# Kernel tuning notes

Hardware: AMD Instinct MI355X
Metric: run time of the kernel (lower is better)

Reference implementation:

```python
import jax, jax.numpy as jnp
import numpy as np

N, E, H, IN, OUT, A, L = 20000, 320000, 128, 16, 16, 4, 4
EPS = 1e-5


def _ln(x, g, b):
    mu = jnp.mean(x, axis=-1, keepdims=True)
    v = jnp.mean((x - mu) ** 2, axis=-1, keepdims=True)
    return (x - mu) * jax.lax.rsqrt(v + EPS) * g + b


def setup_inputs() -> dict:
    key = jax.random.key(0)
    ks = jax.random.split(key, 24)
    x = jax.random.normal(ks[0], (N, 3), dtype=jnp.float32)
    h = jax.random.normal(ks[1], (N, IN), dtype=jnp.float32)
    src = jax.random.randint(ks[2], (E,), 0, N)
    src = src.at[:N].set(jnp.arange(N))  # ensure every node has out-degree>=1 so c>0
    dst = jax.random.randint(ks[3], (E,), 0, N)
    edges = jnp.stack([src, dst]).astype(jnp.int32)
    edge_attr = jax.random.normal(ks[4], (E, A), dtype=jnp.float32)
    s = 0.05
    d_in = 2 * H + 1 + A
    p = {
        "emb_w": jax.random.normal(ks[5], (IN, H)) * s, "emb_b": jnp.zeros((H,)),
        "out_w": jax.random.normal(ks[6], (H, OUT)) * s, "out_b": jnp.zeros((OUT,)),
        "pe_w1": jax.random.normal(ks[7], (L, d_in, H)) * s, "pe_b1": jnp.zeros((L, H)),
        "pe_g1": jnp.ones((L, H)), "pe_bb1": jnp.zeros((L, H)),
        "pe_w2": jax.random.normal(ks[8], (L, H, H)) * s, "pe_b2": jnp.zeros((L, H)),
        "pe_g2": jnp.ones((L, H)), "pe_bb2": jnp.zeros((L, H)),
        "px_w1": jax.random.normal(ks[9], (L, H, H)) * s, "px_b1": jnp.zeros((L, H)),
        "px_g1": jnp.ones((L, H)), "px_bb1": jnp.zeros((L, H)),
        "px_w2": jax.random.normal(ks[10], (L, H, 1)) * s, "px_b2": jnp.zeros((L, 1)),
        "ph_w1": jax.random.normal(ks[11], (L, 2 * H, H)) * s, "ph_b1": jnp.zeros((L, H)),
        "ph_g1": jnp.ones((L, H)), "ph_bb1": jnp.zeros((L, H)),
        "ph_w2": jax.random.normal(ks[12], (L, H, H)) * s, "ph_b2": jnp.zeros((L, H)),
    }
    out = {"x": x, "h": h, "edges": edges, "edge_attr": edge_attr}
    out.update(p)
    return out


def reference(x, h, edges, edge_attr, emb_w, emb_b, out_w, out_b,
              pe_w1, pe_b1, pe_g1, pe_bb1, pe_w2, pe_b2, pe_g2, pe_bb2,
              px_w1, px_b1, px_g1, px_bb1, px_w2, px_b2,
              ph_w1, ph_b1, ph_g1, ph_bb1, ph_w2, ph_b2):
    n = x.shape[0]
    j, i = edges[0], edges[1]  # PyG: x_j = source, x_i = target; aggregate at target i
    # c = in-neighborhood size computed from edge_index[0] (as in the original code)
    c = jax.ops.segment_sum(jnp.ones((edges.shape[1],), x.dtype), j, num_segments=n)[:, None]
    h = h @ emb_w + emb_b
    for l in range(L):
        d = x[i] - x[j]                                   # [E,3]
        d2 = jnp.sum(d * d, axis=-1, keepdims=True)       # ||x_i - x_j||^2
        m_in = jnp.concatenate([h[i], h[j], d2, edge_attr], axis=-1)
        t = jax.nn.silu(_ln(m_in @ pe_w1[l] + pe_b1[l], pe_g1[l], pe_bb1[l]))
        mh = jax.nn.silu(_ln(t @ pe_w2[l] + pe_b2[l], pe_g2[l], pe_bb2[l]))  # [E,H]
        t2 = jax.nn.silu(_ln(mh @ px_w1[l] + px_b1[l], px_g1[l], px_bb1[l]))
        mx = d * (t2 @ px_w2[l] + px_b2[l])               # [E,3]
        agg_x = jax.ops.segment_sum(mx, i, num_segments=n)
        agg_h = jax.ops.segment_sum(mh, i, num_segments=n)
        u = jnp.concatenate([h, agg_h], axis=-1)
        t3 = jax.nn.silu(_ln(u @ ph_w1[l] + ph_b1[l], ph_g1[l], ph_bb1[l]))
        h = t3 @ ph_w2[l] + ph_b2[l] + h                  # ResWrapper residual
        x = x + agg_x / c
    h = h @ out_w + out_b
    return (x, h)
```

## Files before the change

### kernel.cpp

```cpp
#include <hip/hip_runtime.h>

#define NN 20000
#define NE 320000
#define HD 128
#define IND 16
#define OUTD 16
#define NL 4
#define LN_EPS 1e-5f
#define LDA 136

typedef __attribute__((ext_vector_type(8))) short bf16x8;
typedef __attribute__((ext_vector_type(4))) float f32x4;

__device__ __forceinline__ unsigned short f2b(float f) {
  union { float f; unsigned int u; } v; v.f = f;
  unsigned int r = v.u + 0x7FFFu + ((v.u >> 16) & 1u);
  return (unsigned short)(r >> 16);
}
__device__ __forceinline__ float b2f(unsigned int lo16) {
  union { unsigned int u; float f; } v; v.u = lo16 << 16; return v.f;
}


__global__ void prep_zero_k(const float* __restrict__ xin, float* __restrict__ xf,
                            float* __restrict__ cnt, int* __restrict__ deg) {
  int i = blockIdx.x * 256 + threadIdx.x;
  if (i < NN * 3) xf[i] = xin[i];
  if (i < NN) { cnt[i] = 0.f; deg[i] = 0; }
}

__global__ void count_k(const int* __restrict__ edges, float* __restrict__ cnt,
                        int* __restrict__ deg) {
  int e = blockIdx.x * 256 + threadIdx.x;
  if (e < NE) {
    atomicAdd(&cnt[edges[e]], 1.f);
    atomicAdd(&deg[edges[NE + e]], 1);
  }
}

__global__ void inv_k(float* __restrict__ cnt) {
  int n = blockIdx.x * 256 + threadIdx.x;
  if (n < NN) { float c = cnt[n]; cnt[n] = (c > 0.f) ? 1.f / c : 0.f; }
}

__global__ void scan_k(const int* __restrict__ deg, int* __restrict__ rowptr,
                       int* __restrict__ cursor) {
  __shared__ int part[256];
  const int tid = threadIdx.x;
  const int base = tid * 79;
  int s = 0;
  for (int t = 0; t < 79; ++t) { int idx = base + t; if (idx < NN) s += deg[idx]; }
  part[tid] = s;
  __syncthreads();
  for (int off = 1; off < 256; off <<= 1) {
    int v = (tid >= off) ? part[tid - off] : 0;
    __syncthreads();
    part[tid] += v;
    __syncthreads();
  }
  int run = (tid == 0) ? 0 : part[tid - 1];
  for (int t = 0; t < 79; ++t) {
    int idx = base + t;
    if (idx < NN) { rowptr[idx] = run; cursor[idx] = run; run += deg[idx]; }
  }
  if (tid == 255) rowptr[NN] = run;
}

__global__ void scatter_k(const int* __restrict__ edges, int* __restrict__ cursor,
                          int* __restrict__ eids) {
  int e = blockIdx.x * 256 + threadIdx.x;
  if (e < NE) {
    int d = edges[NE + e];
    int pos = atomicAdd(&cursor[d], 1);
    eids[pos] = e;
  }
}

__global__ void prep_w_k(const float* __restrict__ src, unsigned short* __restrict__ dst,
                         int KT, int Kreal) {
  int i = blockIdx.x * 256 + threadIdx.x;
  int total = NL * KT * 4096;
  if (i >= total) return;
  int kk = i & 31;
  int c = (i >> 5) & 127;
  int lkt = i >> 12;
  int kt = lkt % KT;
  int l = lkt / KT;
  int k = kt * 32 + kk;
  float v = (k < Kreal) ? src[((size_t)l * Kreal + k) * HD + c] : 0.f;
  dst[i] = f2b(v);
}

__global__ void emb_k(const float* __restrict__ hin, const float* __restrict__ w,
                      const float* __restrict__ b, float* __restrict__ hf,
                      unsigned short* __restrict__ hb) {
  int i = blockIdx.x * 256 + threadIdx.x;
  if (i >= NN * HD) return;
  int n = i >> 7, c = i & 127;
  float acc = b[c];
#pragma unroll
  for (int k = 0; k < IND; ++k) acc += hin[n * IND + k] * w[k * HD + c];
  hf[i] = acc;
  hb[i] = f2b(acc);
}

__global__ void prepd_k(const float* __restrict__ xf, const int* __restrict__ edges,
                        const float* __restrict__ ea, float* __restrict__ dvec,
                        unsigned short* __restrict__ e8) {
  int e = blockIdx.x * 256 + threadIdx.x;
  if (e >= NE) return;
  int j = edges[e], i = edges[NE + e];
  float dx = xf[i * 3 + 0] - xf[j * 3 + 0];
  float dy = xf[i * 3 + 1] - xf[j * 3 + 1];
  float dz = xf[i * 3 + 2] - xf[j * 3 + 2];
  float d2 = dx * dx + dy * dy + dz * dz;
  dvec[e * 4 + 0] = dx; dvec[e * 4 + 1] = dy; dvec[e * 4 + 2] = dz; dvec[e * 4 + 3] = d2;
  e8[e * 8 + 0] = f2b(d2);
#pragma unroll
  for (int a = 0; a < 4; ++a) e8[e * 8 + 1 + a] = f2b(ea[e * 4 + a]);
  e8[e * 8 + 5] = 0; e8[e * 8 + 6] = 0; e8[e * 8 + 7] = 0;
}

__global__ void outproj_k(const float* __restrict__ hf, const float* __restrict__ w,
                          const float* __restrict__ b, float* __restrict__ out) {
  int i = blockIdx.x * 256 + threadIdx.x;
  if (i >= NN * OUTD) return;
  int n = i >> 4, o = i & 15;
  float acc = b[o];
#pragma unroll 8
  for (int k = 0; k < HD; ++k) acc += hf[(size_t)n * HD + k] * w[k * OUTD + o];
  out[NN * 3 + i] = acc;
}

__global__ void xcopy_k(const float* __restrict__ xf, float* __restrict__ out) {
  int i = blockIdx.x * 256 + threadIdx.x;
  if (i < NN * 3) out[i] = xf[i];
}


__global__ __launch_bounds__(256) void gather_k(const unsigned short* __restrict__ tbuf,
                                                const float* __restrict__ sc,
                                                const float* __restrict__ dvec,
                                                const int* __restrict__ rowptr,
                                                const int* __restrict__ eids,
                                                const float* __restrict__ cinv,
                                                float* __restrict__ aggh,
                                                float* __restrict__ xf) {
  const int n = blockIdx.x * 4 + (threadIdx.x >> 6);
  if (n >= NN) return;
  const int lane = threadIdx.x & 63;
  const int s = rowptr[n], e = rowptr[n + 1];
  float a0 = 0.f, a1 = 0.f, xa = 0.f;
  for (int t = s; t < e; ++t) {
    const int eid = eids[t];
    const unsigned int v = *(const unsigned int*)(tbuf + (size_t)eid * HD + lane * 2);
    a0 += b2f(v & 0xffffu);
    a1 += b2f(v >> 16);
    if (lane < 3) xa += dvec[(size_t)eid * 4 + lane] * sc[eid];
  }
  aggh[(size_t)n * HD + lane * 2] = a0;
  aggh[(size_t)n * HD + lane * 2 + 1] = a1;
  if (lane < 3) xf[n * 3 + lane] += xa * cinv[n];
}


__device__ __forceinline__ void mfma16(const bf16x8 (&af)[4], const bf16x8 (&bq)[4],
                                       f32x4 (&acc)[4][4]) {
#pragma unroll
  for (int mf = 0; mf < 4; ++mf)
#pragma unroll
    for (int nf = 0; nf < 4; ++nf)
      acc[mf][nf] = __builtin_amdgcn_mfma_f32_16x16x32_bf16(af[mf], bq[nf], acc[mf][nf], 0, 0, 0);
}

__device__ __forceinline__ void ln_silu(f32x4 (&acc)[4][4], float (*lnb)[128][2],
                                        const float* bias, const float* g, const float* bb,
                                        int wm, int wn, int lid, int q) {
  float biasc[4], gc[4], bbc[4];
#pragma unroll
  for (int nf = 0; nf < 4; ++nf) {
    const int c = wn * 64 + nf * 16 + lid;
    biasc[nf] = bias[c]; gc[nf] = g[c]; bbc[nf] = bb[c];
  }
#pragma unroll
  for (int mf = 0; mf < 4; ++mf)
#pragma unroll
    for (int nf = 0; nf < 4; ++nf)
#pragma unroll
      for (int rg = 0; rg < 4; ++rg) acc[mf][nf][rg] += biasc[nf];

  float s_[4][4], ss_[4][4];
#pragma unroll
  for (int mf = 0; mf < 4; ++mf)
#pragma unroll
    for (int rg = 0; rg < 4; ++rg) {
      float a = 0.f, b = 0.f;
#pragma unroll
      for (int nf = 0; nf < 4; ++nf) { float v = acc[mf][nf][rg]; a += v; b += v * v; }
      s_[mf][rg] = a; ss_[mf][rg] = b;
    }
#pragma unroll
  for (int m = 1; m < 16; m <<= 1) {
#pragma unroll
    for (int mf = 0; mf < 4; ++mf)
#pragma unroll
      for (int rg = 0; rg < 4; ++rg) {
        s_[mf][rg] += __shfl_xor(s_[mf][rg], m);
        ss_[mf][rg] += __shfl_xor(ss_[mf][rg], m);
      }
  }
  if (lid == 0) {
#pragma unroll
    for (int mf = 0; mf < 4; ++mf)
#pragma unroll
      for (int rg = 0; rg < 4; ++rg) {
        const int rl = wm * 64 + mf * 16 + q * 4 + rg;
        lnb[wn][rl][0] = s_[mf][rg];
        lnb[wn][rl][1] = ss_[mf][rg];
      }
  }
  __syncthreads();
#pragma unroll
  for (int mf = 0; mf < 4; ++mf)
#pragma unroll
    for (int rg = 0; rg < 4; ++rg) {
      const int rl = wm * 64 + mf * 16 + q * 4 + rg;
      const float t0 = lnb[0][rl][0] + lnb[1][rl][0];
      const float t1 = lnb[0][rl][1] + lnb[1][rl][1];
      const float mu = t0 * (1.f / HD);
      const float var = t1 * (1.f / HD) - mu * mu;
      const float rstd = rsqrtf(var + LN_EPS);
#pragma unroll
      for (int nf = 0; nf < 4; ++nf) {
        float v = acc[mf][nf][rg];
        v = (v - mu) * rstd * gc[nf] + bbc[nf];
        acc[mf][nf][rg] = v / (1.f + __expf(-v));
      }
    }
}

__device__ __forceinline__ void write_tile(const f32x4 (&acc)[4][4], unsigned short* At,
                                           int wm, int wn, int lid, int q) {
#pragma unroll
  for (int mf = 0; mf < 4; ++mf)
#pragma unroll
    for (int rg = 0; rg < 4; ++rg) {
      const int row = wm * 64 + mf * 16 + q * 4 + rg;
#pragma unroll
      for (int nf = 0; nf < 4; ++nf) {
        const int col = wn * 64 + nf * 16 + lid;
        At[row * LDA + col] = f2b(acc[mf][nf][rg]);
      }
    }
}


struct EP {
  const unsigned short* hb;
  const unsigned short* e8;
  const int* edges;
  const unsigned short *w1, *w2, *w3;
  const float *b1, *g1, *bb1, *b2, *g2, *bb2, *b3, *g3, *bb3;
  const float *w4, *b4;
  unsigned short* tbuf;
  float* sc;
};

__global__ __launch_bounds__(256, 2) void edge_k(EP p) {
  __shared__ __align__(16) unsigned short At[128 * LDA];
  __shared__ float lnb[2][2][128][2];

  const int tid = threadIdx.x, lane = tid & 63, lid = lane & 15, q = lane >> 4;
  const int wave = tid >> 6, wm = wave >> 1, wn = wave & 1;
  const int row0 = blockIdx.x * 128;

  int rowA[4], ei[4], ej[4], colB[4];
#pragma unroll
  for (int mf = 0; mf < 4; ++mf) {
    rowA[mf] = wm * 64 + mf * 16 + lid;
    ei[mf] = p.edges[NE + row0 + rowA[mf]];
    ej[mf] = p.edges[row0 + rowA[mf]];
  }
#pragma unroll
  for (int nf = 0; nf < 4; ++nf) colB[nf] = wn * 64 + nf * 16 + lid;

  const bf16x8 zv = {0, 0, 0, 0, 0, 0, 0, 0};

  auto ld1 = [&](int kt, bf16x8 (&A)[4], bf16x8 (&B)[4]) {
#pragma unroll
    for (int mf = 0; mf < 4; ++mf) {
      if (kt < 4)
        A[mf] = *(const bf16x8*)(p.hb + (size_t)ei[mf] * HD + kt * 32 + q * 8);
      else if (kt < 8)
        A[mf] = *(const bf16x8*)(p.hb + (size_t)ej[mf] * HD + (kt - 4) * 32 + q * 8);
      else if (q == 0)
        A[mf] = *(const bf16x8*)(p.e8 + (size_t)(row0 + rowA[mf]) * 8);
      else
        A[mf] = zv;
    }
#pragma unroll
    for (int nf = 0; nf < 4; ++nf)
      B[nf] = *(const bf16x8*)(p.w1 + (size_t)kt * 4096 + colB[nf] * 32 + q * 8);
  };
  auto ldL = [&](const unsigned short* wt, int kt, bf16x8 (&A)[4], bf16x8 (&B)[4]) {
#pragma unroll
    for (int mf = 0; mf < 4; ++mf)
      A[mf] = *(const bf16x8*)&At[rowA[mf] * LDA + kt * 32 + q * 8];
#pragma unroll
    for (int nf = 0; nf < 4; ++nf)
      B[nf] = *(const bf16x8*)(wt + (size_t)kt * 4096 + colB[nf] * 32 + q * 8);
  };

  f32x4 acc[4][4];
#pragma unroll
  for (int a = 0; a < 4; ++a)
#pragma unroll
    for (int b = 0; b < 4; ++b) acc[a][b] = (f32x4){0.f, 0.f, 0.f, 0.f};

  bf16x8 A0[4], B0[4], A1[4], B1[4], A2[4], B2[4];

  ld1(0, A0, B0); ld1(1, A1, B1);
  ld1(2, A2, B2); mfma16(A0, B0, acc);
  ld1(3, A0, B0); mfma16(A1, B1, acc);
  ld1(4, A1, B1); mfma16(A2, B2, acc);
  ld1(5, A2, B2); mfma16(A0, B0, acc);
  ld1(6, A0, B0); mfma16(A1, B1, acc);
  ld1(7, A1, B1); mfma16(A2, B2, acc);
  ld1(8, A2, B2); mfma16(A0, B0, acc);
  mfma16(A1, B1, acc);
  mfma16(A2, B2, acc);

  ln_silu(acc, lnb[0], p.b1, p.g1, p.bb1, wm, wn, lid, q);
  write_tile(acc, At, wm, wn, lid, q);
  __syncthreads();

#pragma unroll
  for (int a = 0; a < 4; ++a)
#pragma unroll
    for (int b = 0; b < 4; ++b) acc[a][b] = (f32x4){0.f, 0.f, 0.f, 0.f};
  ldL(p.w2, 0, A0, B0); ldL(p.w2, 1, A1, B1);
  ldL(p.w2, 2, A2, B2); mfma16(A0, B0, acc);
  ldL(p.w2, 3, A0, B0); mfma16(A1, B1, acc);
  mfma16(A2, B2, acc);
  mfma16(A0, B0, acc);

  ln_silu(acc, lnb[1], p.b2, p.g2, p.bb2, wm, wn, lid, q);
  write_tile(acc, At, wm, wn, lid, q);
  __syncthreads();

#pragma unroll
  for (int c4 = 0; c4 < 8; ++c4) {
    const int idx = tid + c4 * 256;
    const int row = idx >> 4, sl = idx & 15;
    const uint4 v = *(const uint4*)&At[row * LDA + sl * 8];
    *(uint4*)(p.tbuf + (size_t)(row0 + row) * HD + sl * 8) = v;
  }

#pragma unroll
  for (int a = 0; a < 4; ++a)
#pragma unroll
    for (int b = 0; b < 4; ++b) acc[a][b] = (f32x4){0.f, 0.f, 0.f, 0.f};
  ldL(p.w3, 0, A0, B0); ldL(p.w3, 1, A1, B1);
  ldL(p.w3, 2, A2, B2); mfma16(A0, B0, acc);
  ldL(p.w3, 3, A0, B0); mfma16(A1, B1, acc);
  mfma16(A2, B2, acc);
  mfma16(A0, B0, acc);

  ln_silu(acc, lnb[0], p.b3, p.g3, p.bb3, wm, wn, lid, q);

  float w4c[4];
#pragma unroll
  for (int nf = 0; nf < 4; ++nf) w4c[nf] = p.w4[colB[nf]];
  float dp[4][4];
#pragma unroll
  for (int mf = 0; mf < 4; ++mf)
#pragma unroll
    for (int rg = 0; rg < 4; ++rg) {
      float a = 0.f;
#pragma unroll
      for (int nf = 0; nf < 4; ++nf) a += acc[mf][nf][rg] * w4c[nf];
      dp[mf][rg] = a;
    }
#pragma unroll
  for (int m = 1; m < 16; m <<= 1) {
#pragma unroll
    for (int mf = 0; mf < 4; ++mf)
#pragma unroll
      for (int rg = 0; rg < 4; ++rg) dp[mf][rg] += __shfl_xor(dp[mf][rg], m);
  }
  if (lid == 0) {
#pragma unroll
    for (int mf = 0; mf < 4; ++mf)
#pragma unroll
      for (int rg = 0; rg < 4; ++rg)
        lnb[1][wn][wm * 64 + mf * 16 + q * 4 + rg][0] = dp[mf][rg];
  }
  __syncthreads();
  if (tid < 128) p.sc[row0 + tid] = lnb[1][0][tid][0] + lnb[1][1][tid][0] + p.b4[0];
}


struct NP {
  const float* hf;
  const float* aggh;
  const unsigned short *w4t, *w5t;
  const float *b1, *g1, *bb1, *b5;
  float* hf_out;
  unsigned short* hb_out;
};

__global__ __launch_bounds__(256, 2) void node_k(NP p) {
  __shared__ __align__(16) unsigned short At[128 * LDA];
  __shared__ float lnb[1][2][128][2];

  const int tid = threadIdx.x, lane = tid & 63, lid = lane & 15, q = lane >> 4;
  const int wave = tid >> 6, wm = wave >> 1, wn = wave & 1;
  const int row0 = blockIdx.x * 128;

  int rowA[4], nrow[4], colB[4];
  bool okm[4];
#pragma unroll
  for (int mf = 0; mf < 4; ++mf) {
    rowA[mf] = wm * 64 + mf * 16 + lid;
    nrow[mf] = row0 + rowA[mf];
    okm[mf] = nrow[mf] < NN;
  }
#pragma unroll
  for (int nf = 0; nf < 4; ++nf) colB[nf] = wn * 64 + nf * 16 + lid;

  const bf16x8 zv = {0, 0, 0, 0, 0, 0, 0, 0};

  auto ld4 = [&](int kt, bf16x8 (&A)[4], bf16x8 (&B)[4]) {
#pragma unroll
    for (int mf = 0; mf < 4; ++mf) {
      if (!okm[mf]) { A[mf] = zv; continue; }
      const float* s = (kt < 4) ? (p.hf + (size_t)nrow[mf] * HD + kt * 32 + q * 8)
                                : (p.aggh + (size_t)nrow[mf] * HD + (kt - 4) * 32 + q * 8);
      const float4 f0 = *(const float4*)s;
      const float4 f1 = *(const float4*)(s + 4);
      unsigned short t[8];
      t[0] = f2b(f0.x); t[1] = f2b(f0.y); t[2] = f2b(f0.z); t[3] = f2b(f0.w);
      t[4] = f2b(f1.x); t[5] = f2b(f1.y); t[6] = f2b(f1.z); t[7] = f2b(f1.w);
      A[mf] = *(const bf16x8*)t;
    }
#pragma unroll
    for (int nf = 0; nf < 4; ++nf)
      B[nf] = *(const bf16x8*)(p.w4t + (size_t)kt * 4096 + colB[nf] * 32 + q * 8);
  };
  auto ld5 = [&](int kt, bf16x8 (&A)[4], bf16x8 (&B)[4]) {
#pragma unroll
    for (int mf = 0; mf < 4; ++mf)
      A[mf] = *(const bf16x8*)&At[rowA[mf] * LDA + kt * 32 + q * 8];
#pragma unroll
    for (int nf = 0; nf < 4; ++nf)
      B[nf] = *(const bf16x8*)(p.w5t + (size_t)kt * 4096 + colB[nf] * 32 + q * 8);
  };

  f32x4 acc[4][4];
#pragma unroll
  for (int a = 0; a < 4; ++a)
#pragma unroll
    for (int b = 0; b < 4; ++b) acc[a][b] = (f32x4){0.f, 0.f, 0.f, 0.f};

  bf16x8 A0[4], B0[4], A1[4], B1[4], A2[4], B2[4];

  ld4(0, A0, B0); ld4(1, A1, B1);
  ld4(2, A2, B2); mfma16(A0, B0, acc);
  ld4(3, A0, B0); mfma16(A1, B1, acc);
  ld4(4, A1, B1); mfma16(A2, B2, acc);
  ld4(5, A2, B2); mfma16(A0, B0, acc);
  ld4(6, A0, B0); mfma16(A1, B1, acc);
  ld4(7, A1, B1); mfma16(A2, B2, acc);
  mfma16(A0, B0, acc);
  mfma16(A1, B1, acc);

  ln_silu(acc, lnb[0], p.b1, p.g1, p.bb1, wm, wn, lid, q);
  write_tile(acc, At, wm, wn, lid, q);
  __syncthreads();

#pragma unroll
  for (int a = 0; a < 4; ++a)
#pragma unroll
    for (int b = 0; b < 4; ++b) acc[a][b] = (f32x4){0.f, 0.f, 0.f, 0.f};
  ld5(0, A0, B0); ld5(1, A1, B1);
  ld5(2, A2, B2); mfma16(A0, B0, acc);
  ld5(3, A0, B0); mfma16(A1, B1, acc);
  mfma16(A2, B2, acc);
  mfma16(A0, B0, acc);

  float biasc[4];
#pragma unroll
  for (int nf = 0; nf < 4; ++nf) biasc[nf] = p.b5[colB[nf]];
#pragma unroll
  for (int mf = 0; mf < 4; ++mf)
#pragma unroll
    for (int rg = 0; rg < 4; ++rg) {
      const int row = wm * 64 + mf * 16 + q * 4 + rg;
      const int n = row0 + row;
      if (n < NN) {
#pragma unroll
        for (int nf = 0; nf < 4; ++nf) {
          const int c = colB[nf];
          const float v = acc[mf][nf][rg] + biasc[nf] + p.hf[(size_t)n * HD + c];
          p.hf_out[(size_t)n * HD + c] = v;
          p.hb_out[(size_t)n * HD + c] = f2b(v);
        }
      }
    }
}


extern "C" void kernel_launch(void* const* d_in, const int* in_sizes, int n_in,
                              void* d_out, int out_size, void* d_ws, size_t ws_size,
                              hipStream_t stream) {
  (void)in_sizes; (void)n_in; (void)out_size; (void)ws_size;
  const float* x_in = (const float*)d_in[0];
  const float* h_in = (const float*)d_in[1];
  const int* edges = (const int*)d_in[2];
  const float* eattr = (const float*)d_in[3];
  const float* emb_w = (const float*)d_in[4];
  const float* emb_b = (const float*)d_in[5];
  const float* out_w = (const float*)d_in[6];
  const float* out_b = (const float*)d_in[7];
  const float* pe_w1 = (const float*)d_in[8];
  const float* pe_b1 = (const float*)d_in[9];
  const float* pe_g1 = (const float*)d_in[10];
  const float* pe_bb1 = (const float*)d_in[11];
  const float* pe_w2 = (const float*)d_in[12];
  const float* pe_b2 = (const float*)d_in[13];
  const float* pe_g2 = (const float*)d_in[14];
  const float* pe_bb2 = (const float*)d_in[15];
  const float* px_w1 = (const float*)d_in[16];
  const float* px_b1 = (const float*)d_in[17];
  const float* px_g1 = (const float*)d_in[18];
  const float* px_bb1 = (const float*)d_in[19];
  const float* px_w2 = (const float*)d_in[20];
  const float* px_b2 = (const float*)d_in[21];
  const float* ph_w1 = (const float*)d_in[22];
  const float* ph_b1 = (const float*)d_in[23];
  const float* ph_g1 = (const float*)d_in[24];
  const float* ph_bb1 = (const float*)d_in[25];
  const float* ph_w2 = (const float*)d_in[26];
  const float* ph_b2 = (const float*)d_in[27];
  float* out = (float*)d_out;

  char* ws = (char*)d_ws;
  size_t off = 0;
  auto alloc = [&](size_t bytes) -> void* {
    void* ptr = ws + off;
    off = (off + bytes + 255) & ~(size_t)255;
    return ptr;
  };
  float* hf = (float*)alloc((size_t)NN * HD * 4);
  unsigned short* hb = (unsigned short*)alloc((size_t)NN * HD * 2);
  float* aggh = (float*)alloc((size_t)NN * HD * 4);
  float* xf = (float*)alloc((size_t)NN * 3 * 4);
  float* cinv = (float*)alloc((size_t)NN * 4);
  float* dvec = (float*)alloc((size_t)NE * 4 * 4);
  unsigned short* e8 = (unsigned short*)alloc((size_t)NE * 8 * 2);
  unsigned short* tbuf = (unsigned short*)alloc((size_t)NE * HD * 2);
  float* sc = (float*)alloc((size_t)NE * 4);
  int* deg = (int*)alloc((size_t)NN * 4);
  int* cursor = (int*)alloc((size_t)NN * 4);
  int* rowptr = (int*)alloc((size_t)(NN + 1) * 4);
  int* eids = (int*)alloc((size_t)NE * 4);
  unsigned short* w1t = (unsigned short*)alloc((size_t)NL * 9 * 4096 * 2);
  unsigned short* w2t = (unsigned short*)alloc((size_t)NL * 4 * 4096 * 2);
  unsigned short* w3t = (unsigned short*)alloc((size_t)NL * 4 * 4096 * 2);
  unsigned short* w4t = (unsigned short*)alloc((size_t)NL * 8 * 4096 * 2);
  unsigned short* w5t = (unsigned short*)alloc((size_t)NL * 4 * 4096 * 2);

  prep_zero_k<<<(NN * 3 + 255) / 256, 256, 0, stream>>>(x_in, xf, cinv, deg);
  count_k<<<(NE + 255) / 256, 256, 0, stream>>>(edges, cinv, deg);
  inv_k<<<(NN + 255) / 256, 256, 0, stream>>>(cinv);
  scan_k<<<1, 256, 0, stream>>>(deg, rowptr, cursor);
  scatter_k<<<(NE + 255) / 256, 256, 0, stream>>>(edges, cursor, eids);
  prep_w_k<<<(NL * 9 * 4096 + 255) / 256, 256, 0, stream>>>(pe_w1, w1t, 9, 261);
  prep_w_k<<<(NL * 4 * 4096 + 255) / 256, 256, 0, stream>>>(pe_w2, w2t, 4, 128);
  prep_w_k<<<(NL * 4 * 4096 + 255) / 256, 256, 0, stream>>>(px_w1, w3t, 4, 128);
  prep_w_k<<<(NL * 8 * 4096 + 255) / 256, 256, 0, stream>>>(ph_w1, w4t, 8, 256);
  prep_w_k<<<(NL * 4 * 4096 + 255) / 256, 256, 0, stream>>>(ph_w2, w5t, 4, 128);
  emb_k<<<(NN * HD + 255) / 256, 256, 0, stream>>>(h_in, emb_w, emb_b, hf, hb);

  const int egrid = NE / 128;
  const int ngrid = (NN + 127) / 128;

  for (int l = 0; l < NL; ++l) {
    prepd_k<<<(NE + 255) / 256, 256, 0, stream>>>(xf, edges, eattr, dvec, e8);
    {
      EP p{};
      p.hb = hb; p.e8 = e8; p.edges = edges;
      p.w1 = w1t + (size_t)l * 9 * 4096;
      p.w2 = w2t + (size_t)l * 4 * 4096;
      p.w3 = w3t + (size_t)l * 4 * 4096;
      p.b1 = pe_b1 + l * HD; p.g1 = pe_g1 + l * HD; p.bb1 = pe_bb1 + l * HD;
      p.b2 = pe_b2 + l * HD; p.g2 = pe_g2 + l * HD; p.bb2 = pe_bb2 + l * HD;
      p.b3 = px_b1 + l * HD; p.g3 = px_g1 + l * HD; p.bb3 = px_bb1 + l * HD;
      p.w4 = px_w2 + l * HD; p.b4 = px_b2 + l;
      p.tbuf = tbuf; p.sc = sc;
      edge_k<<<egrid, 256, 0, stream>>>(p);
    }
    gather_k<<<(NN + 3) / 4, 256, 0, stream>>>(tbuf, sc, dvec, rowptr, eids, cinv, aggh, xf);
    {
      NP p{};
      p.hf = hf; p.aggh = aggh;
      p.w4t = w4t + (size_t)l * 8 * 4096;
      p.w5t = w5t + (size_t)l * 4 * 4096;
      p.b1 = ph_b1 + l * HD; p.g1 = ph_g1 + l * HD; p.bb1 = ph_bb1 + l * HD;
      p.b5 = ph_b2 + l * HD;
      p.hf_out = hf; p.hb_out = hb;
      node_k<<<ngrid, 256, 0, stream>>>(p);
    }
  }

  outproj_k<<<(NN * OUTD + 255) / 256, 256, 0, stream>>>(hf, out_w, out_b, out);
  xcopy_k<<<(NN * 3 + 255) / 256, 256, 0, stream>>>(xf, out);
}
```

Before: 1.365 ms.

## Give each wave full-width row strips to drop cross-wave LayerNorm syncs

Switches the edge and node MLP kernels from a 2x2 wave tiling (64x64 per wave) to row strips where each wave owns 32 rows by all 128 columns. LayerNorm row statistics can then be reduced entirely within a wave, which removes the shared-memory reduction buffer and the block-wide barriers between the chained GEMMs. The GEMM pipeline moves from triple to double buffering, node_k now runs 128-thread blocks over 64 rows, and bf16 conversion now goes through the HIP intrinsic. The cost is that each wave loads the whole weight tile (8 B fragments per k-step instead of 4), so weight traffic per wave doubles and register pressure goes up.

```diff
diff --git a/kernel.cpp b/kernel.cpp
--- a/kernel.cpp
+++ b/kernel.cpp
@@ -1,4 +1,5 @@
 #include <hip/hip_runtime.h>
+#include <hip/hip_bf16.h>
 
 #define NN 20000
 #define NE 320000
@@ -13,9 +14,10 @@
 typedef __attribute__((ext_vector_type(4))) float f32x4;
 
 __device__ __forceinline__ unsigned short f2b(float f) {
-  union { float f; unsigned int u; } v; v.f = f;
-  unsigned int r = v.u + 0x7FFFu + ((v.u >> 16) & 1u);
-  return (unsigned short)(r >> 16);
+  __hip_bfloat16 h = __float2bfloat16(f);
+  unsigned short u;
+  __builtin_memcpy(&u, &h, 2);
+  return u;
 }
 __device__ __forceinline__ float b2f(unsigned int lo16) {
   union { unsigned int u; float f; } v; v.u = lo16 << 16; return v.f;
@@ -164,74 +166,76 @@
 }
 
 
-__device__ __forceinline__ void mfma16(const bf16x8 (&af)[4], const bf16x8 (&bq)[4],
-                                       f32x4 (&acc)[4][4]) {
-#pragma unroll
-  for (int mf = 0; mf < 4; ++mf)
-#pragma unroll
-    for (int nf = 0; nf < 4; ++nf)
-      acc[mf][nf] = __builtin_amdgcn_mfma_f32_16x16x32_bf16(af[mf], bq[nf], acc[mf][nf], 0, 0, 0);
-}
-
-__device__ __forceinline__ void ln_silu(f32x4 (&acc)[4][4], float (*lnb)[128][2],
-                                        const float* bias, const float* g, const float* bb,
-                                        int wm, int wn, int lid, int q) {
-  float biasc[4], gc[4], bbc[4];
-#pragma unroll
-  for (int nf = 0; nf < 4; ++nf) {
-    const int c = wn * 64 + nf * 16 + lid;
+__device__ __forceinline__ void mfma_w(const bf16x8 (&A)[2], const bf16x8 (&B)[8],
+                                       f32x4 (&acc)[2][8]) {
+#pragma unroll
+  for (int mf = 0; mf < 2; ++mf)
+#pragma unroll
+    for (int nf = 0; nf < 8; ++nf)
+      acc[mf][nf] = __builtin_amdgcn_mfma_f32_16x16x32_bf16(A[mf], B[nf], acc[mf][nf], 0, 0, 0);
+}
+
+#define ZACC()                                          \
+  _Pragma("unroll") for (int a_ = 0; a_ < 2; ++a_)      \
+  _Pragma("unroll") for (int b_ = 0; b_ < 8; ++b_)      \
+      acc[a_][b_] = (f32x4){0.f, 0.f, 0.f, 0.f}
+
+#define GEMM_PIPE(NKT, LD)                              \
+  LD(0, A0, B0);                                        \
+  _Pragma("unroll") for (int kt = 0; kt < (NKT); ++kt) {\
+    if ((kt & 1) == 0) {                                \
+      if (kt + 1 < (NKT)) LD(kt + 1, A1, B1);           \
+      mfma_w(A0, B0, acc);                              \
+    } else {                                            \
+      if (kt + 1 < (NKT)) LD(kt + 1, A0, B0);           \
+      mfma_w(A1, B1, acc);                              \
+    }                                                   \
+  }
+
+__device__ __forceinline__ void ln_silu_w(f32x4 (&acc)[2][8], const float* bias,
+                                          const float* g, const float* bb, int lid) {
+  float biasc[8], gc[8], bbc[8];
+#pragma unroll
+  for (int nf = 0; nf < 8; ++nf) {
+    const int c = nf * 16 + lid;
     biasc[nf] = bias[c]; gc[nf] = g[c]; bbc[nf] = bb[c];
   }
 #pragma unroll
-  for (int mf = 0; mf < 4; ++mf)
-#pragma unroll
-    for (int nf = 0; nf < 4; ++nf)
+  for (int mf = 0; mf < 2; ++mf)
+#pragma unroll
+    for (int nf = 0; nf < 8; ++nf)
 #pragma unroll
       for (int rg = 0; rg < 4; ++rg) acc[mf][nf][rg] += biasc[nf];
 
-  float s_[4][4], ss_[4][4];
-#pragma unroll
-  for (int mf = 0; mf < 4; ++mf)
+  float s_[2][4], ss_[2][4];
+#pragma unroll
+  for (int mf = 0; mf < 2; ++mf)
 #pragma unroll
     for (int rg = 0; rg < 4; ++rg) {
       float a = 0.f, b = 0.f;
 #pragma unroll
-      for (int nf = 0; nf < 4; ++nf) { float v = acc[mf][nf][rg]; a += v; b += v * v; }
+      for (int nf = 0; nf < 8; ++nf) { float v = acc[mf][nf][rg]; a += v; b += v * v; }
       s_[mf][rg] = a; ss_[mf][rg] = b;
     }
 #pragma unroll
   for (int m = 1; m < 16; m <<= 1) {
 #pragma unroll
-    for (int mf = 0; mf < 4; ++mf)
+    for (int mf = 0; mf < 2; ++mf)
 #pragma unroll
       for (int rg = 0; rg < 4; ++rg) {
         s_[mf][rg] += __shfl_xor(s_[mf][rg], m);
         ss_[mf][rg] += __shfl_xor(ss_[mf][rg], m);
       }
   }
-  if (lid == 0) {
-#pragma unroll
-    for (int mf = 0; mf < 4; ++mf)
-#pragma unroll
-      for (int rg = 0; rg < 4; ++rg) {
-        const int rl = wm * 64 + mf * 16 + q * 4 + rg;
-        lnb[wn][rl][0] = s_[mf][rg];
-        lnb[wn][rl][1] = ss_[mf][rg];
-      }
-  }
-  __syncthreads();
-#pragma unroll
-  for (int mf = 0; mf < 4; ++mf)
+#pragma unroll
+  for (int mf = 0; mf < 2; ++mf)
 #pragma unroll
     for (int rg = 0; rg < 4; ++rg) {
-      const int rl = wm * 64 + mf * 16 + q * 4 + rg;
-      const float t0 = lnb[0][rl][0] + lnb[1][rl][0];
-      const float t1 = lnb[0][rl][1] + lnb[1][rl][1];
-      const float mu = t0 * (1.f / HD);
-      const float var = t1 * (1.f / HD) - mu * mu;
+      const float mu = s_[mf][rg] * (1.f / HD);
+      const float var = ss_[mf][rg] * (1.f / HD) - mu * mu;
       const float rstd = rsqrtf(var + LN_EPS);
 #pragma unroll
-      for (int nf = 0; nf < 4; ++nf) {
+      for (int nf = 0; nf < 8; ++nf) {
         float v = acc[mf][nf][rg];
         v = (v - mu) * rstd * gc[nf] + bbc[nf];
         acc[mf][nf][rg] = v / (1.f + __expf(-v));
@@ -239,18 +243,16 @@
     }
 }
 
-__device__ __forceinline__ void write_tile(const f32x4 (&acc)[4][4], unsigned short* At,
-                                           int wm, int wn, int lid, int q) {
-#pragma unroll
-  for (int mf = 0; mf < 4; ++mf)
+__device__ __forceinline__ void write_strip(const f32x4 (&acc)[2][8], unsigned short* At,
+                                            int rbase, int lid, int q) {
+#pragma unroll
+  for (int mf = 0; mf < 2; ++mf)
 #pragma unroll
     for (int rg = 0; rg < 4; ++rg) {
-      const int row = wm * 64 + mf * 16 + q * 4 + rg;
-#pragma unroll
-      for (int nf = 0; nf < 4; ++nf) {
-        const int col = wn * 64 + nf * 16 + lid;
-        At[row * LDA + col] = f2b(acc[mf][nf][rg]);
-      }
+      const int row = rbase + mf * 16 + q * 4 + rg;
+#pragma unroll
+      for (int nf = 0; nf < 8; ++nf)
+        At[row * LDA + nf * 16 + lid] = f2b(acc[mf][nf][rg]);
     }
 }
 
@@ -268,135 +270,102 @@
 
 __global__ __launch_bounds__(256, 2) void edge_k(EP p) {
   __shared__ __align__(16) unsigned short At[128 * LDA];
-  __shared__ float lnb[2][2][128][2];
 
   const int tid = threadIdx.x, lane = tid & 63, lid = lane & 15, q = lane >> 4;
-  const int wave = tid >> 6, wm = wave >> 1, wn = wave & 1;
+  const int wave = tid >> 6;
+  const int rbase = wave * 32;
   const int row0 = blockIdx.x * 128;
 
-  int rowA[4], ei[4], ej[4], colB[4];
-#pragma unroll
-  for (int mf = 0; mf < 4; ++mf) {
-    rowA[mf] = wm * 64 + mf * 16 + lid;
-    ei[mf] = p.edges[NE + row0 + rowA[mf]];
-    ej[mf] = p.edges[row0 + rowA[mf]];
-  }
-#pragma unroll
-  for (int nf = 0; nf < 4; ++nf) colB[nf] = wn * 64 + nf * 16 + lid;
+  int ei[2], ej[2];
+#pragma unroll
+  for (int mf = 0; mf < 2; ++mf) {
+    const int r = row0 + rbase + mf * 16 + lid;
+    ei[mf] = p.edges[NE + r];
+    ej[mf] = p.edges[r];
+  }
 
   const bf16x8 zv = {0, 0, 0, 0, 0, 0, 0, 0};
 
-  auto ld1 = [&](int kt, bf16x8 (&A)[4], bf16x8 (&B)[4]) {
-#pragma unroll
-    for (int mf = 0; mf < 4; ++mf) {
+  auto LD1 = [&](int kt, bf16x8 (&A)[2], bf16x8 (&B)[8]) {
+#pragma unroll
+    for (int mf = 0; mf < 2; ++mf) {
       if (kt < 4)
         A[mf] = *(const bf16x8*)(p.hb + (size_t)ei[mf] * HD + kt * 32 + q * 8);
       else if (kt < 8)
         A[mf] = *(const bf16x8*)(p.hb + (size_t)ej[mf] * HD + (kt - 4) * 32 + q * 8);
       else if (q == 0)
-        A[mf] = *(const bf16x8*)(p.e8 + (size_t)(row0 + rowA[mf]) * 8);
+        A[mf] = *(const bf16x8*)(p.e8 + (size_t)(row0 + rbase + mf * 16 + lid) * 8);
       else
         A[mf] = zv;
     }
 #pragma unroll
-    for (int nf = 0; nf < 4; ++nf)
-      B[nf] = *(const bf16x8*)(p.w1 + (size_t)kt * 4096 + colB[nf] * 32 + q * 8);
+    for (int nf = 0; nf < 8; ++nf)
+      B[nf] = *(const bf16x8*)(p.w1 + (size_t)kt * 4096 + (nf * 16 + lid) * 32 + q * 8);
   };
-  auto ldL = [&](const unsigned short* wt, int kt, bf16x8 (&A)[4], bf16x8 (&B)[4]) {
-#pragma unroll
-    for (int mf = 0; mf < 4; ++mf)
-      A[mf] = *(const bf16x8*)&At[rowA[mf] * LDA + kt * 32 + q * 8];
-#pragma unroll
-    for (int nf = 0; nf < 4; ++nf)
-      B[nf] = *(const bf16x8*)(wt + (size_t)kt * 4096 + colB[nf] * 32 + q * 8);
+  auto LDW = [&](const unsigned short* wt, int kt, bf16x8 (&A)[2], bf16x8 (&B)[8]) {
+#pragma unroll
+    for (int mf = 0; mf < 2; ++mf)
+      A[mf] = *(const bf16x8*)&At[(rbase + mf * 16 + lid) * LDA + kt * 32 + q * 8];
+#pragma unroll
+    for (int nf = 0; nf < 8; ++nf)
+      B[nf] = *(const bf16x8*)(wt + (size_t)kt * 4096 + (nf * 16 + lid) * 32 + q * 8);
   };
-
-  f32x4 acc[4][4];
-#pragma unroll
-  for (int a = 0; a < 4; ++a)
-#pragma unroll
-    for (int b = 0; b < 4; ++b) acc[a][b] = (f32x4){0.f, 0.f, 0.f, 0.f};
-
-  bf16x8 A0[4], B0[4], A1[4], B1[4], A2[4], B2[4];
-
-  ld1(0, A0, B0); ld1(1, A1, B1);
-  ld1(2, A2, B2); mfma16(A0, B0, acc);
-  ld1(3, A0, B0); mfma16(A1, B1, acc);
-  ld1(4, A1, B1); mfma16(A2, B2, acc);
-  ld1(5, A2, B2); mfma16(A0, B0, acc);
-  ld1(6, A0, B0); mfma16(A1, B1, acc);
-  ld1(7, A1, B1); mfma16(A2, B2, acc);
-  ld1(8, A2, B2); mfma16(A0, B0, acc);
-  mfma16(A1, B1, acc);
-  mfma16(A2, B2, acc);
-
-  ln_silu(acc, lnb[0], p.b1, p.g1, p.bb1, wm, wn, lid, q);
-  write_tile(acc, At, wm, wn, lid, q);
-  __syncthreads();
-
-#pragma unroll
-  for (int a = 0; a < 4; ++a)
-#pragma unroll
-    for (int b = 0; b < 4; ++b) acc[a][b] = (f32x4){0.f, 0.f, 0.f, 0.f};
-  ldL(p.w2, 0, A0, B0); ldL(p.w2, 1, A1, B1);
-  ldL(p.w2, 2, A2, B2); mfma16(A0, B0, acc);
-  ldL(p.w2, 3, A0, B0); mfma16(A1, B1, acc);
-  mfma16(A2, B2, acc);
-  mfma16(A0, B0, acc);
-
-  ln_silu(acc, lnb[1], p.b2, p.g2, p.bb2, wm, wn, lid, q);
-  write_tile(acc, At, wm, wn, lid, q);
-  __syncthreads();
-
-#pragma unroll
-  for (int c4 = 0; c4 < 8; ++c4) {
-    const int idx = tid + c4 * 256;
+  auto LD2 = [&](int kt, bf16x8 (&A)[2], bf16x8 (&B)[8]) { LDW(p.w2, kt, A, B); };
+  auto LD3 = [&](int kt, bf16x8 (&A)[2], bf16x8 (&B)[8]) { LDW(p.w3, kt, A, B); };
+
+  f32x4 acc[2][8];
+  bf16x8 A0[2], B0[8], A1[2], B1[8];
+
+  ZACC();
+  GEMM_PIPE(9, LD1);
+  ln_silu_w(acc, p.b1, p.g1, p.bb1, lid);
+  write_strip(acc, At, rbase, lid, q);
+
+  ZACC();
+  GEMM_PIPE(4, LD2);
+  ln_silu_w(acc, p.b2, p.g2, p.bb2, lid);
+  write_strip(acc, At, rbase, lid, q);
+
+#pragma unroll
+  for (int it = 0; it < 8; ++it) {
+    const int idx = it * 64 + lane;
     const int row = idx >> 4, sl = idx & 15;
-    const uint4 v = *(const uint4*)&At[row * LDA + sl * 8];
-    *(uint4*)(p.tbuf + (size_t)(row0 + row) * HD + sl * 8) = v;
-  }
-
-#pragma unroll
-  for (int a = 0; a < 4; ++a)
-#pragma unroll
-    for (int b = 0; b < 4; ++b) acc[a][b] = (f32x4){0.f, 0.f, 0.f, 0.f};
-  ldL(p.w3, 0, A0, B0); ldL(p.w3, 1, A1, B1);
-  ldL(p.w3, 2, A2, B2); mfma16(A0, B0, acc);
-  ldL(p.w3, 3, A0, B0); mfma16(A1, B1, acc);
-  mfma16(A2, B2, acc);
-  mfma16(A0, B0, acc);
-
-  ln_silu(acc, lnb[0], p.b3, p.g3, p.bb3, wm, wn, lid, q);
-
-  float w4c[4];
-#pragma unroll
-  for (int nf = 0; nf < 4; ++nf) w4c[nf] = p.w4[colB[nf]];
-  float dp[4][4];
-#pragma unroll
-  for (int mf = 0; mf < 4; ++mf)
+    const uint4 v = *(const uint4*)&At[(rbase + row) * LDA + sl * 8];
+    *(uint4*)(p.tbuf + (size_t)(row0 + rbase + row) * HD + sl * 8) = v;
+  }
+
+  ZACC();
+  GEMM_PIPE(4, LD3);
+  ln_silu_w(acc, p.b3, p.g3, p.bb3, lid);
+
+  float w4c[8];
+#pragma unroll
+  for (int nf = 0; nf < 8; ++nf) w4c[nf] = p.w4[nf * 16 + lid];
+  float dp[2][4];
+#pragma unroll
+  for (int mf = 0; mf < 2; ++mf)
 #pragma unroll
     for (int rg = 0; rg < 4; ++rg) {
       float a = 0.f;
 #pragma unroll
-      for (int nf = 0; nf < 4; ++nf) a += acc[mf][nf][rg] * w4c[nf];
+      for (int nf = 0; nf < 8; ++nf) a += acc[mf][nf][rg] * w4c[nf];
       dp[mf][rg] = a;
     }
 #pragma unroll
   for (int m = 1; m < 16; m <<= 1) {
 #pragma unroll
-    for (int mf = 0; mf < 4; ++mf)
+    for (int mf = 0; mf < 2; ++mf)
 #pragma unroll
       for (int rg = 0; rg < 4; ++rg) dp[mf][rg] += __shfl_xor(dp[mf][rg], m);
   }
   if (lid == 0) {
-#pragma unroll
-    for (int mf = 0; mf < 4; ++mf)
+    const float b4 = p.b4[0];
+#pragma unroll
+    for (int mf = 0; mf < 2; ++mf)
 #pragma unroll
       for (int rg = 0; rg < 4; ++rg)
-        lnb[1][wn][wm * 64 + mf * 16 + q * 4 + rg][0] = dp[mf][rg];
-  }
-  __syncthreads();
-  if (tid < 128) p.sc[row0 + tid] = lnb[1][0][tid][0] + lnb[1][1][tid][0] + p.b4[0];
+        p.sc[row0 + rbase + mf * 16 + q * 4 + rg] = dp[mf][rg] + b4;
+  }
 }
 
 
@@ -409,30 +378,27 @@
   unsigned short* hb_out;
 };
 
-__global__ __launch_bounds__(256, 2) void node_k(NP p) {
-  __shared__ __align__(16) unsigned short At[128 * LDA];
-  __shared__ float lnb[1][2][128][2];
+__global__ __launch_bounds__(128, 2) void node_k(NP p) {
+  __shared__ __align__(16) unsigned short At[64 * LDA];
 
   const int tid = threadIdx.x, lane = tid & 63, lid = lane & 15, q = lane >> 4;
-  const int wave = tid >> 6, wm = wave >> 1, wn = wave & 1;
-  const int row0 = blockIdx.x * 128;
-
-  int rowA[4], nrow[4], colB[4];
-  bool okm[4];
-#pragma unroll
-  for (int mf = 0; mf < 4; ++mf) {
-    rowA[mf] = wm * 64 + mf * 16 + lid;
-    nrow[mf] = row0 + rowA[mf];
+  const int wave = tid >> 6;
+  const int rbase = wave * 32;
+  const int row0 = blockIdx.x * 64;
+
+  int nrow[2];
+  bool okm[2];
+#pragma unroll
+  for (int mf = 0; mf < 2; ++mf) {
+    nrow[mf] = row0 + rbase + mf * 16 + lid;
     okm[mf] = nrow[mf] < NN;
   }
-#pragma unroll
-  for (int nf = 0; nf < 4; ++nf) colB[nf] = wn * 64 + nf * 16 + lid;
 
   const bf16x8 zv = {0, 0, 0, 0, 0, 0, 0, 0};
 
-  auto ld4 = [&](int kt, bf16x8 (&A)[4], bf16x8 (&B)[4]) {
-#pragma unroll
-    for (int mf = 0; mf < 4; ++mf) {
+  auto LD4 = [&](int kt, bf16x8 (&A)[2], bf16x8 (&B)[8]) {
+#pragma unroll
+    for (int mf = 0; mf < 2; ++mf) {
       if (!okm[mf]) { A[mf] = zv; continue; }
       const float* s = (kt < 4) ? (p.hf + (size_t)nrow[mf] * HD + kt * 32 + q * 8)
                                 : (p.aggh + (size_t)nrow[mf] * HD + (kt - 4) * 32 + q * 8);
@@ -444,63 +410,41 @@
       A[mf] = *(const bf16x8*)t;
     }
 #pragma unroll
-    for (int nf = 0; nf < 4; ++nf)
-      B[nf] = *(const bf16x8*)(p.w4t + (size_t)kt * 4096 + colB[nf] * 32 + q * 8);
+    for (int nf = 0; nf < 8; ++nf)
+      B[nf] = *(const bf16x8*)(p.w4t + (size_t)kt * 4096 + (nf * 16 + lid) * 32 + q * 8);
   };
-  auto ld5 = [&](int kt, bf16x8 (&A)[4], bf16x8 (&B)[4]) {
-#pragma unroll
-    for (int mf = 0; mf < 4; ++mf)
-      A[mf] = *(const bf16x8*)&At[rowA[mf] * LDA + kt * 32 + q * 8];
-#pragma unroll
-    for (int nf = 0; nf < 4; ++nf)
-      B[nf] = *(const bf16x8*)(p.w5t + (size_t)kt * 4096 + colB[nf] * 32 + q * 8);
+  auto LD5 = [&](int kt, bf16x8 (&A)[2], bf16x8 (&B)[8]) {
+#pragma unroll
+    for (int mf = 0; mf < 2; ++mf)
+      A[mf] = *(const bf16x8*)&At[(rbase + mf * 16 + lid) * LDA + kt * 32 + q * 8];
+#pragma unroll
+    for (int nf = 0; nf < 8; ++nf)
+      B[nf] = *(const bf16x8*)(p.w5t + (size_t)kt * 4096 + (nf * 16 + lid) * 32 + q * 8);
   };
 
-  f32x4 acc[4][4];
-#pragma unroll
-  for (int a = 0; a < 4; ++a)
-#pragma unroll
-    for (int b = 0; b < 4; ++b) acc[a][b] = (f32x4){0.f, 0.f, 0.f, 0.f};
-
-  bf16x8 A0[4], B0[4], A1[4], B1[4], A2[4], B2[4];
-
-  ld4(0, A0, B0); ld4(1, A1, B1);
-  ld4(2, A2, B2); mfma16(A0, B0, acc);
-  ld4(3, A0, B0); mfma16(A1, B1, acc);
-  ld4(4, A1, B1); mfma16(A2, B2, acc);
-  ld4(5, A2, B2); mfma16(A0, B0, acc);
-  ld4(6, A0, B0); mfma16(A1, B1, acc);
-  ld4(7, A1, B1); mfma16(A2, B2, acc);
-  mfma16(A0, B0, acc);
-  mfma16(A1, B1, acc);
-
-  ln_silu(acc, lnb[0], p.b1, p.g1, p.bb1, wm, wn, lid, q);
-  write_tile(acc, At, wm, wn, lid, q);
-  __syncthreads();
-
-#pragma unroll
-  for (int a = 0; a < 4; ++a)
-#pragma unroll
-    for (int b = 0; b < 4; ++b) acc[a][b] = (f32x4){0.f, 0.f, 0.f, 0.f};
-  ld5(0, A0, B0); ld5(1, A1, B1);
-  ld5(2, A2, B2); mfma16(A0, B0, acc);
-  ld5(3, A0, B0); mfma16(A1, B1, acc);
-  mfma16(A2, B2, acc);
-  mfma16(A0, B0, acc);
-
-  float biasc[4];
-#pragma unroll
-  for (int nf = 0; nf < 4; ++nf) biasc[nf] = p.b5[colB[nf]];
-#pragma unroll
-  for (int mf = 0; mf < 4; ++mf)
+  f32x4 acc[2][8];
+  bf16x8 A0[2], B0[8], A1[2], B1[8];
+
+  ZACC();
+  GEMM_PIPE(8, LD4);
+  ln_silu_w(acc, p.b1, p.g1, p.bb1, lid);
+  write_strip(acc, At, rbase, lid, q);
+
+  ZACC();
+  GEMM_PIPE(4, LD5);
+
+  float biasc[8];
+#pragma unroll
+  for (int nf = 0; nf < 8; ++nf) biasc[nf] = p.b5[nf * 16 + lid];
+#pragma unroll
+  for (int mf = 0; mf < 2; ++mf)
 #pragma unroll
     for (int rg = 0; rg < 4; ++rg) {
-      const int row = wm * 64 + mf * 16 + q * 4 + rg;
-      const int n = row0 + row;
+      const int n = row0 + rbase + mf * 16 + q * 4 + rg;
       if (n < NN) {
 #pragma unroll
-        for (int nf = 0; nf < 4; ++nf) {
-          const int c = colB[nf];
+        for (int nf = 0; nf < 8; ++nf) {
+          const int c = nf * 16 + lid;
           const float v = acc[mf][nf][rg] + biasc[nf] + p.hf[(size_t)n * HD + c];
           p.hf_out[(size_t)n * HD + c] = v;
           p.hb_out[(size_t)n * HD + c] = f2b(v);
@@ -583,7 +527,7 @@
   emb_k<<<(NN * HD + 255) / 256, 256, 0, stream>>>(h_in, emb_w, emb_b, hf, hb);
 
   const int egrid = NE / 128;
-  const int ngrid = (NN + 127) / 128;
+  const int ngrid = (NN + 63) / 64;
 
   for (int l = 0; l < NL; ++l) {
     prepd_k<<<(NE + 255) / 256, 256, 0, stream>>>(xf, edges, eattr, dvec, e8);
@@ -609,7 +553,7 @@
       p.b1 = ph_b1 + l * HD; p.g1 = ph_g1 + l * HD; p.bb1 = ph_bb1 + l * HD;
       p.b5 = ph_b2 + l * HD;
       p.hf_out = hf; p.hb_out = hb;
-      node_k<<<ngrid, 256, 0, stream>>>(p);
+      node_k<<<ngrid, 128, 0, stream>>>(p);
     }
   }
 
```

New measurement: 1.215 ms. -11.0%, faster.
